# Performance work log

Measured on AMD Instinct MI355X. Metric: run time of the kernel, lower is better.

Reference implementation:

```python
import jax, jax.numpy as jnp
import numpy as np

N, E, B, D, Q, C = 50000, 250000, 128, 302, 600, 2000
NEG_SLOPE = 0.2  # PyG GATConv default


def setup_inputs() -> dict:
    key = jax.random.key(0)
    ks = jax.random.split(key, 12)
    x = jax.random.normal(ks[0], (N, D), jnp.float32)
    edges = jax.random.randint(ks[1], (2, E), 0, N, dtype=jnp.int32)
    query = jax.random.normal(ks[2], (B, Q), jnp.float32)
    batch = jnp.sort(jax.random.randint(ks[3], (N,), 0, B, dtype=jnp.int32))
    # GATConv(302, 302, heads=1) params (shared across the 3 applications)
    theta = jax.random.normal(ks[4], (D, D), jnp.float32) / np.float32(np.sqrt(D))
    att_src = jax.random.normal(ks[5], (D,), jnp.float32) * 0.1
    att_dst = jax.random.normal(ks[6], (D,), jnp.float32) * 0.1
    gat_bias = jnp.zeros((D,), jnp.float32)
    # Attention.W ~ torch.rand(decoder_dim, encoder_dim) -> stored as [Q, D]
    attW = jax.random.uniform(ks[7], (Q, D), jnp.float32)
    lin_w = jax.random.normal(ks[8], (C, D), jnp.float32) / np.float32(np.sqrt(D))
    lin_b = jnp.zeros((C,), jnp.float32)
    return {"x": x, "edges": edges, "query": query, "batch": batch,
            "theta": theta, "att_src": att_src, "att_dst": att_dst,
            "gat_bias": gat_bias, "attW": attW, "lin_w": lin_w, "lin_b": lin_b}


def _segment_softmax(s, seg, num_segments):
    m = jax.ops.segment_max(s, seg, num_segments=num_segments)
    ex = jnp.exp(s - m[seg])
    den = jax.ops.segment_sum(ex, seg, num_segments=num_segments)
    return ex / den[seg]


def reference(x, edges, query, batch, theta, att_src, att_dst, gat_bias, attW, lin_w, lin_b):
    # add self loops once (PyG GATConv add_self_loops=True)
    loops = jnp.arange(N, dtype=edges.dtype)
    src = jnp.concatenate([edges[0], loops])
    dst = jnp.concatenate([edges[1], loops])

    def gat(h_in):
        h = h_in @ theta.T                       # [N, D]
        a_s = h @ att_src                        # [N]
        a_d = h @ att_dst                        # [N]
        e = jax.nn.leaky_relu(a_s[src] + a_d[dst], NEG_SLOPE)  # [E+N]
        alpha = _segment_softmax(e, dst, N)      # softmax over incoming edges
        out = jax.ops.segment_sum(alpha[:, None] * h[src], dst, num_segments=N)
        return out + gat_bias

    h = jax.nn.relu(gat(x))
    h = jax.nn.relu(gat(h))
    h = jax.nn.relu(gat(h))                      # [N, D]

    # Attention pooling: score_j = (query[batch_j] @ W) . h_j / sqrt(Q)
    qp = query @ attW                            # [B, D]
    s = jnp.sum(qp[batch] * h, axis=-1) / np.float32(np.sqrt(Q))  # [N]
    w = _segment_softmax(s, batch, B)            # per-graph softmax weights
    pooled = jax.ops.segment_sum(w[:, None] * h, batch, num_segments=B)  # [B, D]

    return jax.nn.relu(pooled) @ lin_w.T + lin_b  # [B, C]
```

## Files before the change

kernel.cpp:

```cpp
#include <hip/hip_runtime.h>
#include <hip/hip_bf16.h>
#include <math.h>

#define N_NODES 50000
#define N_EDGES 250000
#define BB      128
#define DD      302
#define QQ      600
#define CC      2000
#define NEG_SLOPE 0.2f
#define GS      304
#define KP      320
#define KSTEPS  10
#define PC      64
#define BPK_KS  20480

typedef __attribute__((ext_vector_type(8))) short short8;
typedef __attribute__((ext_vector_type(4))) float f32x4;

__device__ __forceinline__ void gload_lds16(const void* g, void* l) {
    __builtin_amdgcn_global_load_lds((const __attribute__((address_space(1))) void*)g,
                                     (__attribute__((address_space(3))) void*)l, 16, 0, 0);
}

__device__ __host__ __forceinline__ int bswz(int q, int n) {
    return q ^ (n & 3) ^ ((n >> 2) & 3);
}

__device__ __forceinline__ unsigned short f2bf(float v) {
    return (unsigned short)((__float_as_uint(v) + 0x8000u) >> 16);
}

__global__ void k_zero_dc(int* deg, int* cursor) {
    int i = blockIdx.x * 256 + threadIdx.x;
    if (i < N_NODES) { deg[i] = 0; cursor[i] = 0; }
}

__global__ void k_histogram(const int* __restrict__ dst, int* deg) {
    int e = blockIdx.x * blockDim.x + threadIdx.x;
    if (e < N_EDGES) atomicAdd(&deg[dst[e]], 1);
}

__global__ void k_scan_block(const int* __restrict__ deg, int* offs, int* partials) {
    __shared__ int sh[256];
    int i = blockIdx.x * 256 + threadIdx.x;
    int v = (i < N_NODES) ? deg[i] : 0;
    sh[threadIdx.x] = v;
    __syncthreads();
    for (int d = 1; d < 256; d <<= 1) {
        int t = (threadIdx.x >= d) ? sh[threadIdx.x - d] : 0;
        __syncthreads();
        sh[threadIdx.x] += t;
        __syncthreads();
    }
    if (i < N_NODES) offs[i] = sh[threadIdx.x] - v;
    if (threadIdx.x == 255) partials[blockIdx.x] = sh[255];
}

__global__ void k_scan_partials(int* partials, int nb) {
    __shared__ int sh[256];
    int v = (threadIdx.x < nb) ? partials[threadIdx.x] : 0;
    sh[threadIdx.x] = v;
    __syncthreads();
    for (int d = 1; d < 256; d <<= 1) {
        int t = (threadIdx.x >= d) ? sh[threadIdx.x - d] : 0;
        __syncthreads();
        sh[threadIdx.x] += t;
        __syncthreads();
    }
    if (threadIdx.x < nb) partials[threadIdx.x] = sh[threadIdx.x] - v;
}

__global__ void k_scatter(const int* __restrict__ src, const int* __restrict__ dst,
                          const int* __restrict__ offs, const int* __restrict__ partials,
                          const int* __restrict__ deg, int* cursor, int* esrc) {
    int i = blockIdx.x * blockDim.x + threadIdx.x;
    if (i < N_EDGES) {
        int d = dst[i];
        int base = offs[d] + partials[d >> 8] + d;
        int pos = base + atomicAdd(&cursor[d], 1);
        esrc[pos] = src[i];
    } else if (i < N_EDGES + N_NODES) {
        int n = i - N_EDGES;
        int base = offs[n] + partials[n >> 8] + n;
        esrc[base + deg[n]] = n;
    }
}

__global__ void k_theta_qp(const float* __restrict__ theta,
                           const float* __restrict__ att_src,
                           const float* __restrict__ att_dst,
                           unsigned short* __restrict__ bpk,
                           const float* __restrict__ query,
                           const float* __restrict__ attW,
                           float* __restrict__ qp) {
    if (blockIdx.x >= 402) {
        int t = blockIdx.x - 402;
        int b = t >> 1;
        int d = (t & 1) * 256 + threadIdx.x;
        if (d >= DD) return;
        const float* qrow = query + (size_t)b * QQ;
        float acc = 0.f;
        #pragma unroll 8
        for (int q = 0; q < QQ; q++) acc += qrow[q] * attW[(size_t)q * DD + d];
        qp[(size_t)b * DD + d] = acc;
        return;
    }
    if (blockIdx.x >= 400) {
        int k = (blockIdx.x - 400) * 256 + threadIdx.x;
        if (k >= KP) return;
        float vs = 0.f, vd = 0.f;
        if (k < DD) {
            for (int j = 0; j < DD; j++) {
                float t = theta[j * DD + k];
                vs += t * att_src[j];
                vd += t * att_dst[j];
            }
        }
        int ks = k >> 5, kk = k & 31, q = kk >> 3, kb = kk & 7;
        size_t b0 = (size_t)ks * BPK_KS + DD * 32 + bswz(q, DD) * 8 + kb;
        size_t b1 = (size_t)ks * BPK_KS + (DD + 1) * 32 + bswz(q, DD + 1) * 8 + kb;
        unsigned int u, uh, ul;
        u  = __float_as_uint(vs);
        uh = (u + 0x8000u) & 0xffff0000u;
        ul = (__float_as_uint(vs - __uint_as_float(uh)) + 0x8000u) >> 16;
        bpk[b0]         = (unsigned short)(uh >> 16);
        bpk[b0 + 10240] = (unsigned short)ul;
        u  = __float_as_uint(vd);
        uh = (u + 0x8000u) & 0xffff0000u;
        ul = (__float_as_uint(vd - __uint_as_float(uh)) + 0x8000u) >> 16;
        bpk[b1]         = (unsigned short)(uh >> 16);
        bpk[b1 + 10240] = (unsigned short)ul;
        return;
    }
    int idx = blockIdx.x * 256 + threadIdx.x;
    if (idx >= KP * KP) return;
    int n = idx / KP, k = idx % KP;
    if (n == DD || n == DD + 1) return;
    float v = (n < DD && k < DD) ? theta[n * DD + k] : 0.f;
    unsigned int u  = __float_as_uint(v);
    unsigned int uh = (u + 0x8000u) & 0xffff0000u;
    float hf = __uint_as_float(uh);
    float lo = v - hf;
    unsigned int ul = (__float_as_uint(lo) + 0x8000u) >> 16;
    int ks = k >> 5, kk = k & 31, q = kk >> 3, kb = kk & 7;
    size_t base = (size_t)ks * BPK_KS + n * 32 + bswz(q, n) * 8 + kb;
    bpk[base]         = (unsigned short)(uh >> 16);
    bpk[base + 10240] = (unsigned short)ul;
}

__global__ __launch_bounds__(256) void k_mfma_gemm(const float* __restrict__ A, int lda,
                                                   const unsigned short* __restrict__ Bpk,
                                                   unsigned short* __restrict__ Gb,
                                                   float* __restrict__ a_s,
                                                   float* __restrict__ a_d, int M) {
    __shared__ __attribute__((aligned(16))) unsigned short Bs[2][BPK_KS];

    const int tid   = threadIdx.x;
    const int lane  = tid & 63;
    const int wave  = tid >> 6;
    const int q     = lane >> 4;
    const int mr    = lane & 15;
    const int m0    = blockIdx.x * 64;
    const int nbase = wave * 80;
    const int kvalid = (lda == GS) ? GS : DD;

    f32x4 acc[4][5];
    #pragma unroll
    for (int i = 0; i < 4; i++)
        #pragma unroll
        for (int j = 0; j < 5; j++)
            acc[i][j] = (f32x4){0.f, 0.f, 0.f, 0.f};

    const float* arow[4];
    bool rok[4];
    #pragma unroll
    for (int mt = 0; mt < 4; mt++) {
        int row = m0 + mt * 16 + mr;
        rok[mt]  = row < M;
        arow[mt] = A + (size_t)(row < M ? row : 0) * lda;
    }

    const char* gB = (const char*)Bpk;

    auto loadA = [&](float (&f)[4][8], int ks) {
        const int k0c = ks * 32 + q * 8;
        #pragma unroll
        for (int mt = 0; mt < 4; mt++) {
            if (rok[mt] && (k0c + 8 <= kvalid)) {
                float4 v0 = *(const float4*)(arow[mt] + k0c);
                float4 v1 = *(const float4*)(arow[mt] + k0c + 4);
                f[mt][0]=v0.x; f[mt][1]=v0.y; f[mt][2]=v0.z; f[mt][3]=v0.w;
                f[mt][4]=v1.x; f[mt][5]=v1.y; f[mt][6]=v1.z; f[mt][7]=v1.w;
            } else {
                #pragma unroll
                for (int p = 0; p < 8; p += 2) {
                    int k = k0c + p;
                    float2 t = {0.f, 0.f};
                    if (rok[mt] && k < kvalid) t = *(const float2*)(arow[mt] + k);
                    f[mt][p] = t.x; f[mt][p+1] = t.y;
                }
            }
        }
    };

    auto stageB = [&](int buf, int ks) {
        const char* gsrc = gB + (size_t)(ks * BPK_KS) * 2;
        #pragma unroll
        for (int j = 0; j < 10; j++) {
            int chunk = j * 4 + wave;
            gload_lds16(gsrc + chunk * 1024 + lane * 16,
                        (char*)Bs[buf] + chunk * 1024);
        }
    };

    float fcur[4][8], fnext[4][8];

    loadA(fcur, 0);
    stageB(0, 0);
    __syncthreads();

    #pragma unroll
    for (int ks = 0; ks < KSTEPS; ks++) {
        if (ks + 1 < KSTEPS) {
            stageB((ks + 1) & 1, ks + 1);
            loadA(fnext, ks + 1);
        }

        short8 ah[4], al[4];
        #pragma unroll
        for (int mt = 0; mt < 4; mt++) {
            #pragma unroll
            for (int p = 0; p < 8; p++) {
                unsigned int u  = __float_as_uint(fcur[mt][p]);
                unsigned int uh = (u + 0x8000u) & 0xffff0000u;
                float l = fcur[mt][p] - __uint_as_float(uh);
                ah[mt][p] = (short)(uh >> 16);
                al[mt][p] = (short)((__float_as_uint(l) + 0x8000u) >> 16);
            }
        }

        const unsigned short* Bc = Bs[ks & 1];
        short8 bh[5], bl[5];
        #pragma unroll
        for (int nt = 0; nt < 5; nt++) {
            int col = nbase + nt * 16 + mr;
            int off = col * 32 + bswz(q, col) * 8;
            bh[nt] = *(const short8*)&Bc[off];
            bl[nt] = *(const short8*)&Bc[10240 + off];
        }
        #pragma unroll
        for (int nt = 0; nt < 5; nt++) {
            #pragma unroll
            for (int mt = 0; mt < 4; mt++) {
                acc[mt][nt] = __builtin_amdgcn_mfma_f32_16x16x32_bf16(ah[mt], bh[nt], acc[mt][nt], 0, 0, 0);
                acc[mt][nt] = __builtin_amdgcn_mfma_f32_16x16x32_bf16(ah[mt], bl[nt], acc[mt][nt], 0, 0, 0);
                acc[mt][nt] = __builtin_amdgcn_mfma_f32_16x16x32_bf16(al[mt], bh[nt], acc[mt][nt], 0, 0, 0);
            }
        }

        __syncthreads();

        #pragma unroll
        for (int mt = 0; mt < 4; mt++)
            #pragma unroll
            for (int p = 0; p < 8; p++)
                fcur[mt][p] = fnext[mt][p];
    }

    #pragma unroll
    for (int mt = 0; mt < 4; mt++) {
        int row_b = m0 + mt * 16 + q * 4;
        #pragma unroll
        for (int nt = 0; nt < 5; nt++) {
            int col = nbase + nt * 16 + mr;
            if (col > DD + 1) continue;
            #pragma unroll
            for (int r = 0; r < 4; r++) {
                int row = row_b + r;
                if (row >= M) continue;
                float v = acc[mt][nt][r];
                if (col < DD) {
                    Gb[(size_t)row * GS + col] = f2bf(v);
                } else if (col == DD) {
                    a_s[row] = v;
                    Gb[(size_t)row * GS + DD] = 0;
                } else {
                    a_d[row] = v;
                    Gb[(size_t)row * GS + DD + 1] = 0;
                }
            }
        }
    }
}

#define BM 64
#define BN 64
#define BK 16
__global__ __launch_bounds__(256) void k_gemm_nt(const float* __restrict__ A,
                                                 const float* __restrict__ B,
                                                 float* __restrict__ C,
                                                 int M, int N, int K,
                                                 const float* __restrict__ bias,
                                                 int relu_a) {
    __shared__ float As[BK][BM + 4];
    __shared__ float Bs[BK][BN + 4];
    int m0 = blockIdx.y * BM;
    int n0 = blockIdx.x * BN;
    int tid = threadIdx.x;
    int tr = tid >> 4;
    int tc = tid & 15;
    float acc[4][4] = {};
    for (int k0 = 0; k0 < K; k0 += BK) {
        #pragma unroll
        for (int j = 0; j < 4; j++) {
            int e = tid + 256 * j;
            int r = e >> 4;
            int k = e & 15;
            int gk = k0 + k;
            int gm = m0 + r;
            float va = 0.f;
            if (gm < M && gk < K) va = A[(size_t)gm * K + gk];
            if (relu_a) va = fmaxf(va, 0.f);
            As[k][r] = va;
            int gn = n0 + r;
            float vb = 0.f;
            if (gn < N && gk < K) vb = B[(size_t)gn * K + gk];
            Bs[k][r] = vb;
        }
        __syncthreads();
        #pragma unroll
        for (int k = 0; k < BK; k++) {
            float a[4], b[4];
            #pragma unroll
            for (int i = 0; i < 4; i++) a[i] = As[k][tr * 4 + i];
            #pragma unroll
            for (int j = 0; j < 4; j++) b[j] = Bs[k][tc * 4 + j];
            #pragma unroll
            for (int i = 0; i < 4; i++)
                #pragma unroll
                for (int j = 0; j < 4; j++)
                    acc[i][j] += a[i] * b[j];
        }
        __syncthreads();
    }
    #pragma unroll
    for (int i = 0; i < 4; i++) {
        int gm = m0 + tr * 4 + i;
        if (gm >= M) continue;
        #pragma unroll
        for (int j = 0; j < 4; j++) {
            int gn = n0 + tc * 4 + j;
            if (gn < N) {
                float v = acc[i][j];
                if (bias) v += bias[gn];
                C[(size_t)gm * N + gn] = v;
            }
        }
    }
}

__global__ __launch_bounds__(256) void k_aggregate(const unsigned short* __restrict__ Gb,
                                                   const float* __restrict__ a_s,
                                                   const float* __restrict__ a_d,
                                                   const int* __restrict__ offs,
                                                   const int* __restrict__ partials,
                                                   const int* __restrict__ deg,
                                                   const int* __restrict__ esrc,
                                                   const float* __restrict__ bias,
                                                   float* __restrict__ out,
                                                   const float* __restrict__ qp,
                                                   const int* __restrict__ batch,
                                                   float* __restrict__ sarr) {
    int gid = blockIdx.x * blockDim.x + threadIdx.x;
    int n = gid >> 6, lane = gid & 63;
    if (n >= N_NODES) return;
    int beg = offs[n] + partials[n >> 8] + n;
    int cnt = deg[n] + 1;
    float adn = a_d[n];

    int   s_reg = 0;
    float e_reg = -1.0e30f;
    float m = -1.0e30f, den = 0.f;
    if (lane < cnt) {
        s_reg = esrc[beg + lane];
        float e = a_s[s_reg] + adn;
        e = (e > 0.f) ? e : NEG_SLOPE * e;
        e_reg = e;
        m = e; den = 1.f;
    }
    for (int i = 64 + lane; i < cnt; i += 64) {
        float e = a_s[esrc[beg + i]] + adn;
        e = (e > 0.f) ? e : NEG_SLOPE * e;
        float nm = fmaxf(m, e);
        den = den * __expf(m - nm) + __expf(e - nm);
        m = nm;
    }
    for (int off = 32; off; off >>= 1) {
        float mo = __shfl_xor(m, off);
        float dn = __shfl_xor(den, off);
        float nm = fmaxf(m, mo);
        den = den * __expf(m - nm) + dn * __expf(mo - nm);
        m = nm;
    }
    float inv_den = 1.f / den;
    float w_reg = __expf(e_reg - m) * inv_den;

    const int c0 = lane * 8;
    const bool act = c0 < GS;
    float A8[8] = {0.f,0.f,0.f,0.f,0.f,0.f,0.f,0.f};
    const int nfirst = (cnt < 64) ? cnt : 64;
    #pragma unroll 4
    for (int j = 0; j < nfirst; j++) {
        int   s = __shfl(s_reg, j);
        float w = __shfl(w_reg, j);
        if (act) {
            int4 v = *(const int4*)(Gb + (size_t)s * GS + c0);
            unsigned int u0 = (unsigned int)v.x, u1 = (unsigned int)v.y;
            unsigned int u2 = (unsigned int)v.z, u3 = (unsigned int)v.w;
            A8[0] += w * __uint_as_float(u0 << 16);
            A8[1] += w * __uint_as_float(u0 & 0xffff0000u);
            A8[2] += w * __uint_as_float(u1 << 16);
            A8[3] += w * __uint_as_float(u1 & 0xffff0000u);
            A8[4] += w * __uint_as_float(u2 << 16);
            A8[5] += w * __uint_as_float(u2 & 0xffff0000u);
            A8[6] += w * __uint_as_float(u3 << 16);
            A8[7] += w * __uint_as_float(u3 & 0xffff0000u);
        }
    }
    for (int i = 64; i < cnt; i++) {
        int s = esrc[beg + i];
        float e = a_s[s] + adn;
        e = (e > 0.f) ? e : NEG_SLOPE * e;
        float w = __expf(e - m) * inv_den;
        if (act) {
            int4 v = *(const int4*)(Gb + (size_t)s * GS + c0);
            unsigned int u0 = (unsigned int)v.x, u1 = (unsigned int)v.y;
            unsigned int u2 = (unsigned int)v.z, u3 = (unsigned int)v.w;
            A8[0] += w * __uint_as_float(u0 << 16);
            A8[1] += w * __uint_as_float(u0 & 0xffff0000u);
            A8[2] += w * __uint_as_float(u1 << 16);
            A8[3] += w * __uint_as_float(u1 & 0xffff0000u);
            A8[4] += w * __uint_as_float(u2 << 16);
            A8[5] += w * __uint_as_float(u2 & 0xffff0000u);
            A8[6] += w * __uint_as_float(u3 << 16);
            A8[7] += w * __uint_as_float(u3 & 0xffff0000u);
        }
    }

    float o[8];
    if (act) {
        #pragma unroll
        for (int p = 0; p < 8; p++) {
            int col = c0 + p;
            float b = (col < DD) ? bias[col] : 0.f;
            o[p] = (col < DD) ? fmaxf(A8[p] + b, 0.f) : 0.f;
        }
        float4 w0 = {o[0], o[1], o[2], o[3]};
        float4 w1 = {o[4], o[5], o[6], o[7]};
        *(float4*)(out + (size_t)n * GS + c0)     = w0;
        *(float4*)(out + (size_t)n * GS + c0 + 4) = w1;
    }

    if (sarr) {
        float d = 0.f;
        if (act) {
            const float* qv = qp + (size_t)batch[n] * DD;
            #pragma unroll
            for (int p = 0; p < 8; p++) {
                int col = c0 + p;
                if (col < DD) d += o[p] * qv[col];
            }
        }
        for (int off = 32; off; off >>= 1) d += __shfl_xor(d, off);
        if (lane == 0) sarr[n] = d * 0.04082482904638630f;
    }
}

__global__ __launch_bounds__(256) void k_gstats(const float* __restrict__ sarr,
                                                const int* __restrict__ batch,
                                                float* __restrict__ wn,
                                                float* __restrict__ pooled) {
    int b = blockIdx.x;
    int lo = 0, hi = N_NODES;
    while (lo < hi) { int mid = (lo + hi) >> 1; if (batch[mid] < b) lo = mid + 1; else hi = mid; }
    int beg = lo;
    hi = N_NODES;
    while (lo < hi) { int mid = (lo + hi) >> 1; if (batch[mid] < b + 1) lo = mid + 1; else hi = mid; }
    int cnt = lo - beg;

    __shared__ float red[256];
    float m = -INFINITY;
    for (int i = threadIdx.x; i < cnt; i += 256) m = fmaxf(m, sarr[beg + i]);
    red[threadIdx.x] = m;
    __syncthreads();
    for (int d = 128; d; d >>= 1) {
        if (threadIdx.x < d) red[threadIdx.x] = fmaxf(red[threadIdx.x], red[threadIdx.x + d]);
        __syncthreads();
    }
    m = red[0];
    __syncthreads();
    float den = 0.f;
    for (int i = threadIdx.x; i < cnt; i += 256) den += __expf(sarr[beg + i] - m);
    red[threadIdx.x] = den;
    __syncthreads();
    for (int d = 128; d; d >>= 1) {
        if (threadIdx.x < d) red[threadIdx.x] += red[threadIdx.x + d];
        __syncthreads();
    }
    float dinv = (cnt > 0) ? 1.f / red[0] : 0.f;
    for (int i = threadIdx.x; i < cnt; i += 256)
        wn[beg + i] = __expf(sarr[beg + i] - m) * dinv;
    for (int j = threadIdx.x; j < DD; j += 256)
        pooled[(size_t)b * DD + j] = 0.f;
}

__global__ __launch_bounds__(256) void k_poolacc(const float* __restrict__ h, int ld,
                                                 const float* __restrict__ wn,
                                                 const int* __restrict__ batch,
                                                 float* __restrict__ pooled) {
    int c0 = blockIdx.x * PC;
    if (c0 >= N_NODES) return;
    int nmax = N_NODES - c0; if (nmax > PC) nmax = PC;
    __shared__ int   sb[PC];
    __shared__ float sw[PC];
    for (int i = threadIdx.x; i < nmax; i += 256) {
        sb[i] = batch[c0 + i];
        sw[i] = wn[c0 + i];
    }
    __syncthreads();
    int f0 = threadIdx.x, f1 = threadIdx.x + 256;
    float a0 = 0.f, a1 = 0.f;
    int g = sb[0];
    for (int i = 0; i < nmax; i++) {
        int bi = sb[i];
        if (bi != g) {
            if (f0 < DD) atomicAdd(&pooled[(size_t)g * DD + f0], a0);
            if (f1 < DD) atomicAdd(&pooled[(size_t)g * DD + f1], a1);
            a0 = 0.f; a1 = 0.f; g = bi;
        }
        float w = sw[i];
        const float* row = h + (size_t)(c0 + i) * ld;
        if (f0 < DD) a0 += w * row[f0];
        if (f1 < DD) a1 += w * row[f1];
    }
    if (f0 < DD) atomicAdd(&pooled[(size_t)g * DD + f0], a0);
    if (f1 < DD) atomicAdd(&pooled[(size_t)g * DD + f1], a1);
}

extern "C" void kernel_launch(void* const* d_in, const int* in_sizes, int n_in,
                              void* d_out, int out_size, void* d_ws, size_t ws_size,
                              hipStream_t stream) {
    const float* x        = (const float*)d_in[0];
    const int*   edges    = (const int*)d_in[1];
    const float* query    = (const float*)d_in[2];
    const int*   batch    = (const int*)d_in[3];
    const float* theta    = (const float*)d_in[4];
    const float* att_src  = (const float*)d_in[5];
    const float* att_dst  = (const float*)d_in[6];
    const float* gat_bias = (const float*)d_in[7];
    const float* attW     = (const float*)d_in[8];
    const float* lin_w    = (const float*)d_in[9];
    const float* lin_b    = (const float*)d_in[10];
    float* out = (float*)d_out;

    char* ws = (char*)d_ws;
    size_t off = 0;
    auto alloc = [&](size_t bytes) -> void* {
        off = (off + 255) & ~(size_t)255;
        void* p = ws + off;
        off += bytes;
        return p;
    };

    unsigned short* Gb = (unsigned short*)alloc((size_t)N_NODES * GS * 2);
    float* P    = (float*)alloc((size_t)N_NODES * GS * 4);
    unsigned short* bpk = (unsigned short*)alloc((size_t)KSTEPS * BPK_KS * 2);
    float* a_s  = (float*)alloc((size_t)N_NODES * 4);
    float* a_d  = (float*)alloc((size_t)N_NODES * 4);
    float* sarr = (float*)alloc((size_t)N_NODES * 4);
    float* wn   = (float*)alloc((size_t)N_NODES * 4);
    int* deg    = (int*)alloc((size_t)N_NODES * 4);
    int* cursor = (int*)alloc((size_t)N_NODES * 4);
    int* offs   = (int*)alloc((size_t)N_NODES * 4);
    int* esrc   = (int*)alloc((size_t)(N_EDGES + N_NODES) * 4);
    int* partials = (int*)alloc(256 * 4);
    float* qp   = (float*)alloc((size_t)BB * DD * 4);
    float* pooled = (float*)alloc((size_t)BB * DD * 4);

    const int* e_src = edges;
    const int* e_dst = edges + N_EDGES;

    const int NB_SCAN = (N_NODES + 255) / 256;

    k_zero_dc<<<NB_SCAN, 256, 0, stream>>>(deg, cursor);
    k_histogram<<<(N_EDGES + 255) / 256, 256, 0, stream>>>(e_dst, deg);
    k_scan_block<<<NB_SCAN, 256, 0, stream>>>(deg, offs, partials);
    k_scan_partials<<<1, 256, 0, stream>>>(partials, NB_SCAN);
    k_scatter<<<(N_EDGES + N_NODES + 255) / 256, 256, 0, stream>>>(e_src, e_dst, offs, partials, deg, cursor, esrc);

    k_theta_qp<<<658, 256, 0, stream>>>(theta, att_src, att_dst, bpk, query, attW, qp);

    int mfma_blocks = (N_NODES + 63) / 64;
    int wave_blocks = (N_NODES + 3) / 4;
    const float* cur = x;
    int cur_ld = DD;
    for (int layer = 0; layer < 3; layer++) {
        k_mfma_gemm<<<mfma_blocks, 256, 0, stream>>>(cur, cur_ld, bpk, Gb, a_s, a_d, N_NODES);
        bool last = (layer == 2);
        k_aggregate<<<wave_blocks, 256, 0, stream>>>(Gb, a_s, a_d, offs, partials, deg, esrc, gat_bias, P,
                                                     last ? qp : (const float*)nullptr,
                                                     last ? batch : (const int*)nullptr,
                                                     last ? sarr : (float*)nullptr);
        cur = P;
        cur_ld = GS;
    }

    k_gstats<<<BB, 256, 0, stream>>>(sarr, batch, wn, pooled);
    k_poolacc<<<(N_NODES + PC - 1) / PC, 256, 0, stream>>>(P, GS, wn, batch, pooled);
    {
        dim3 g((CC + BN - 1) / BN, (BB + BM - 1) / BM);
        k_gemm_nt<<<g, 256, 0, stream>>>(pooled, lin_w, out, BB, CC, DD, lin_b, 1);
    }
}
```

Baseline: 646.7 us.

## Store hidden layer activations in bf16 and skip low-part MFMA for layers 2-3

```diff
diff --git a/kernel.cpp b/kernel.cpp
--- a/kernel.cpp
+++ b/kernel.cpp
@@ -29,6 +29,9 @@
 
 __device__ __forceinline__ unsigned short f2bf(float v) {
     return (unsigned short)((__float_as_uint(v) + 0x8000u) >> 16);
+}
+__device__ __forceinline__ float bf2f(unsigned short u) {
+    return __uint_as_float(((unsigned int)u) << 16);
 }
 
 __global__ void k_zero_dc(int* deg, int* cursor) {
@@ -149,7 +152,9 @@
     bpk[base + 10240] = (unsigned short)ul;
 }
 
-__global__ __launch_bounds__(256) void k_mfma_gemm(const float* __restrict__ A, int lda,
+__global__ __launch_bounds__(256) void k_mfma_gemm(const float* __restrict__ A32,
+                                                   const unsigned short* __restrict__ A16,
+                                                   int lda,
                                                    const unsigned short* __restrict__ Bpk,
                                                    unsigned short* __restrict__ Gb,
                                                    float* __restrict__ a_s,
@@ -163,7 +168,7 @@
     const int mr    = lane & 15;
     const int m0    = blockIdx.x * 64;
     const int nbase = wave * 80;
-    const int kvalid = (lda == GS) ? GS : DD;
+    const bool abf  = (A16 != nullptr);
 
     f32x4 acc[4][5];
     #pragma unroll
@@ -172,24 +177,27 @@
         for (int j = 0; j < 5; j++)
             acc[i][j] = (f32x4){0.f, 0.f, 0.f, 0.f};
 
-    const float* arow[4];
+    const float* arow32[4];
+    const unsigned short* arow16[4];
     bool rok[4];
     #pragma unroll
     for (int mt = 0; mt < 4; mt++) {
         int row = m0 + mt * 16 + mr;
-        rok[mt]  = row < M;
-        arow[mt] = A + (size_t)(row < M ? row : 0) * lda;
+        rok[mt] = row < M;
+        int r = row < M ? row : 0;
+        arow32[mt] = abf ? nullptr : (A32 + (size_t)r * lda);
+        arow16[mt] = abf ? (A16 + (size_t)r * GS) : nullptr;
     }
 
     const char* gB = (const char*)Bpk;
 
-    auto loadA = [&](float (&f)[4][8], int ks) {
+    auto loadA32 = [&](float (&f)[4][8], int ks) {
         const int k0c = ks * 32 + q * 8;
         #pragma unroll
         for (int mt = 0; mt < 4; mt++) {
-            if (rok[mt] && (k0c + 8 <= kvalid)) {
-                float4 v0 = *(const float4*)(arow[mt] + k0c);
-                float4 v1 = *(const float4*)(arow[mt] + k0c + 4);
+            if (rok[mt] && (k0c + 8 <= DD)) {
+                float4 v0 = *(const float4*)(arow32[mt] + k0c);
+                float4 v1 = *(const float4*)(arow32[mt] + k0c + 4);
                 f[mt][0]=v0.x; f[mt][1]=v0.y; f[mt][2]=v0.z; f[mt][3]=v0.w;
                 f[mt][4]=v1.x; f[mt][5]=v1.y; f[mt][6]=v1.z; f[mt][7]=v1.w;
             } else {
@@ -197,9 +205,21 @@
                 for (int p = 0; p < 8; p += 2) {
                     int k = k0c + p;
                     float2 t = {0.f, 0.f};
-                    if (rok[mt] && k < kvalid) t = *(const float2*)(arow[mt] + k);
+                    if (rok[mt] && k < DD) t = *(const float2*)(arow32[mt] + k);
                     f[mt][p] = t.x; f[mt][p+1] = t.y;
                 }
+            }
+        }
+    };
+
+    auto loadA16 = [&](short8 (&s)[4], int ks) {
+        const int k0c = ks * 32 + q * 8;
+        #pragma unroll
+        for (int mt = 0; mt < 4; mt++) {
+            if (rok[mt] && (k0c + 8 <= GS)) {
+                s[mt] = *(const short8*)(arow16[mt] + k0c);
+            } else {
+                s[mt] = (short8){0,0,0,0,0,0,0,0};
             }
         }
     };
@@ -215,8 +235,9 @@
     };
 
     float fcur[4][8], fnext[4][8];
-
-    loadA(fcur, 0);
+    short8 scur[4], snext[4];
+
+    if (abf) loadA16(scur, 0); else loadA32(fcur, 0);
     stageB(0, 0);
     __syncthreads();
 
@@ -224,19 +245,24 @@
     for (int ks = 0; ks < KSTEPS; ks++) {
         if (ks + 1 < KSTEPS) {
             stageB((ks + 1) & 1, ks + 1);
-            loadA(fnext, ks + 1);
+            if (abf) loadA16(snext, ks + 1); else loadA32(fnext, ks + 1);
         }
 
         short8 ah[4], al[4];
-        #pragma unroll
-        for (int mt = 0; mt < 4; mt++) {
-            #pragma unroll
-            for (int p = 0; p < 8; p++) {
-                unsigned int u  = __float_as_uint(fcur[mt][p]);
-                unsigned int uh = (u + 0x8000u) & 0xffff0000u;
-                float l = fcur[mt][p] - __uint_as_float(uh);
-                ah[mt][p] = (short)(uh >> 16);
-                al[mt][p] = (short)((__float_as_uint(l) + 0x8000u) >> 16);
+        if (abf) {
+            #pragma unroll
+            for (int mt = 0; mt < 4; mt++) ah[mt] = scur[mt];
+        } else {
+            #pragma unroll
+            for (int mt = 0; mt < 4; mt++) {
+                #pragma unroll
+                for (int p = 0; p < 8; p++) {
+                    unsigned int u  = __float_as_uint(fcur[mt][p]);
+                    unsigned int uh = (u + 0x8000u) & 0xffff0000u;
+                    float l = fcur[mt][p] - __uint_as_float(uh);
+                    ah[mt][p] = (short)(uh >> 16);
+                    al[mt][p] = (short)((__float_as_uint(l) + 0x8000u) >> 16);
+                }
             }
         }
 
@@ -255,17 +281,23 @@
             for (int mt = 0; mt < 4; mt++) {
                 acc[mt][nt] = __builtin_amdgcn_mfma_f32_16x16x32_bf16(ah[mt], bh[nt], acc[mt][nt], 0, 0, 0);
                 acc[mt][nt] = __builtin_amdgcn_mfma_f32_16x16x32_bf16(ah[mt], bl[nt], acc[mt][nt], 0, 0, 0);
-                acc[mt][nt] = __builtin_amdgcn_mfma_f32_16x16x32_bf16(al[mt], bh[nt], acc[mt][nt], 0, 0, 0);
-            }
-        }
-
-        __syncthreads();
-
-        #pragma unroll
-        for (int mt = 0; mt < 4; mt++)
-            #pragma unroll
-            for (int p = 0; p < 8; p++)
-                fcur[mt][p] = fnext[mt][p];
+                if (!abf)
+                    acc[mt][nt] = __builtin_amdgcn_mfma_f32_16x16x32_bf16(al[mt], bh[nt], acc[mt][nt], 0, 0, 0);
+            }
+        }
+
+        __syncthreads();
+
+        if (abf) {
+            #pragma unroll
+            for (int mt = 0; mt < 4; mt++) scur[mt] = snext[mt];
+        } else {
+            #pragma unroll
+            for (int mt = 0; mt < 4; mt++)
+                #pragma unroll
+                for (int p = 0; p < 8; p++)
+                    fcur[mt][p] = fnext[mt][p];
+        }
     }
 
     #pragma unroll
@@ -368,7 +400,7 @@
                                                    const int* __restrict__ deg,
                                                    const int* __restrict__ esrc,
                                                    const float* __restrict__ bias,
-                                                   float* __restrict__ out,
+                                                   unsigned short* __restrict__ Pb,
                                                    const float* __restrict__ qp,
                                                    const int* __restrict__ batch,
                                                    float* __restrict__ sarr) {
@@ -450,16 +482,15 @@
 
     float o[8];
     if (act) {
+        short8 wv;
         #pragma unroll
         for (int p = 0; p < 8; p++) {
             int col = c0 + p;
             float b = (col < DD) ? bias[col] : 0.f;
             o[p] = (col < DD) ? fmaxf(A8[p] + b, 0.f) : 0.f;
-        }
-        float4 w0 = {o[0], o[1], o[2], o[3]};
-        float4 w1 = {o[4], o[5], o[6], o[7]};
-        *(float4*)(out + (size_t)n * GS + c0)     = w0;
-        *(float4*)(out + (size_t)n * GS + c0 + 4) = w1;
+            wv[p] = (short)f2bf(o[p]);
+        }
+        *(short8*)(Pb + (size_t)n * GS + c0) = wv;
     }
 
     if (sarr) {
@@ -515,7 +546,7 @@
         pooled[(size_t)b * DD + j] = 0.f;
 }
 
-__global__ __launch_bounds__(256) void k_poolacc(const float* __restrict__ h, int ld,
+__global__ __launch_bounds__(256) void k_poolacc(const unsigned short* __restrict__ Pb,
                                                  const float* __restrict__ wn,
                                                  const int* __restrict__ batch,
                                                  float* __restrict__ pooled) {
@@ -540,9 +571,9 @@
             a0 = 0.f; a1 = 0.f; g = bi;
         }
         float w = sw[i];
-        const float* row = h + (size_t)(c0 + i) * ld;
-        if (f0 < DD) a0 += w * row[f0];
-        if (f1 < DD) a1 += w * row[f1];
+        const unsigned short* row = Pb + (size_t)(c0 + i) * GS;
+        if (f0 < DD) a0 += w * bf2f(row[f0]);
+        if (f1 < DD) a1 += w * bf2f(row[f1]);
     }
     if (f0 < DD) atomicAdd(&pooled[(size_t)g * DD + f0], a0);
     if (f1 < DD) atomicAdd(&pooled[(size_t)g * DD + f1], a1);
@@ -574,7 +605,7 @@
     };
 
     unsigned short* Gb = (unsigned short*)alloc((size_t)N_NODES * GS * 2);
-    float* P    = (float*)alloc((size_t)N_NODES * GS * 4);
+    unsigned short* Pb = (unsigned short*)alloc((size_t)N_NODES * GS * 2);
     unsigned short* bpk = (unsigned short*)alloc((size_t)KSTEPS * BPK_KS * 2);
     float* a_s  = (float*)alloc((size_t)N_NODES * 4);
     float* a_d  = (float*)alloc((size_t)N_NODES * 4);
@@ -603,21 +634,20 @@
 
     int mfma_blocks = (N_NODES + 63) / 64;
     int wave_blocks = (N_NODES + 3) / 4;
-    const float* cur = x;
-    int cur_ld = DD;
     for (int layer = 0; layer < 3; layer++) {
-        k_mfma_gemm<<<mfma_blocks, 256, 0, stream>>>(cur, cur_ld, bpk, Gb, a_s, a_d, N_NODES);
+        if (layer == 0)
+            k_mfma_gemm<<<mfma_blocks, 256, 0, stream>>>(x, nullptr, DD, bpk, Gb, a_s, a_d, N_NODES);
+        else
+            k_mfma_gemm<<<mfma_blocks, 256, 0, stream>>>(nullptr, Pb, GS, bpk, Gb, a_s, a_d, N_NODES);
         bool last = (layer == 2);
-        k_aggregate<<<wave_blocks, 256, 0, stream>>>(Gb, a_s, a_d, offs, partials, deg, esrc, gat_bias, P,
+        k_aggregate<<<wave_blocks, 256, 0, stream>>>(Gb, a_s, a_d, offs, partials, deg, esrc, gat_bias, Pb,
                                                      last ? qp : (const float*)nullptr,
                                                      last ? batch : (const int*)nullptr,
                                                      last ? sarr : (float*)nullptr);
-        cur = P;
-        cur_ld = GS;
     }
 
     k_gstats<<<BB, 256, 0, stream>>>(sarr, batch, wn, pooled);
-    k_poolacc<<<(N_NODES + PC - 1) / PC, 256, 0, stream>>>(P, GS, wn, batch, pooled);
+    k_poolacc<<<(N_NODES + PC - 1) / PC, 256, 0, stream>>>(Pb, wn, batch, pooled);
     {
         dim3 g((CC + BN - 1) / BN, (BB + BM - 1) / BM);
         k_gemm_nt<<<g, 256, 0, stream>>>(pooled, lin_w, out, BB, CC, DD, lin_b, 1);
```

Measured after the change: 694.4 us. +7.4%, slower.
